# Optimization experiments

Measured on AMD Instinct MI355X. Metric: run time of the kernel, lower is better.

The kernel has to match this reference:

```python
import jax, jax.numpy as jnp
import numpy as np

B = 16          # number of trees (batch)
H = 256         # hidden_size == feature_size
S = 16          # Tree.num_sem
C = 5           # max_child_num (complete C-ary tree)
L = 6           # tree depth: leaves at level L, internal levels 0..L-1
N_LEAF = C**L                     # 15625
N_INT = (C**L - 1) // (C - 1)     # 3906 internal nodes, level-l offset = (C^l-1)/(C-1)


def setup_inputs() -> dict:
    key = jax.random.key(0)
    ks = jax.random.split(key, 20)
    rn = lambda k, shp, s=0.05: jax.random.normal(k, shp, dtype=jnp.float32) * s
    return {
        "leaf_box": jax.random.normal(ks[0], (B, N_LEAF, 4), dtype=jnp.float32),
        "leaf_sem": jax.random.uniform(ks[1], (B, N_LEAF, S), dtype=jnp.float32),
        "internal_box": jax.random.normal(ks[2], (B, N_INT, 4), dtype=jnp.float32),
        "node_type": jax.random.randint(ks[3], (B, N_INT), 0, 3, dtype=jnp.int32),
        "eps": jax.random.normal(ks[4], (B, H), dtype=jnp.float32),
        "W_box": rn(ks[5], (4, H)), "b_box": jnp.zeros((H,), jnp.float32),
        "W_sem": rn(ks[6], (S, H)), "b_sem": jnp.zeros((H,), jnp.float32),
        "W_node": rn(ks[7], (3, C * H, H)), "b_node": jnp.zeros((3, H), jnp.float32),
        "W1": rn(ks[8], (H, H)), "b1": jnp.zeros((H,), jnp.float32),
        "Wmu": rn(ks[9], (H, H)), "bmu": jnp.zeros((H,), jnp.float32),
        "Wvar": rn(ks[10], (H, H)), "bvar": jnp.zeros((H,), jnp.float32),
    }


def reference(leaf_box, leaf_sem, internal_box, node_type, eps,
              W_box, b_box, W_sem, b_sem, W_node, b_node,
              W1, b1, Wmu, bmu, Wvar, bvar):
    box_enc = lambda b: jax.nn.relu(b @ W_box + b_box)
    # LeafEncoder: relu-box-encoding + relu-sem-encoding
    feats = box_enc(leaf_box) + jax.nn.relu(leaf_sem @ W_sem + b_sem)  # [B, N_LEAF, H]
    # Bottom-up over internal levels (static loop over L=6 levels)
    for l in range(L - 1, -1, -1):
        n = C ** l
        off = (C ** l - 1) // (C - 1)
        child = feats.reshape(B, n, C * H)  # children flattened per parent (child_exists==1)
        # Apply all 3 branch encoders (vertical/horizontal/stack), select by node label
        y_all = jnp.einsum('bnk,tkh->bnth', child, W_node) + b_node          # [B,n,3,H]
        sel = jax.nn.one_hot(node_type[:, off:off + n], 3, dtype=child.dtype)  # [B,n,3]
        y = jnp.einsum('bnth,bnt->bnh', y_all, sel)
        feats = jax.nn.relu(y) + box_enc(internal_box[:, off:off + n])
    root = feats[:, 0]  # [B, H]
    # Sampler (variational, probabilistic)
    enc = jax.nn.relu(root @ W1 + b1)
    mu = enc @ Wmu + bmu
    logvar = enc @ Wvar + bvar
    std = jnp.exp(0.5 * logvar)
    kld = 1.0 + logvar - mu ** 2 - jnp.exp(logvar)
    return jnp.concatenate([eps * std + mu, kld], axis=1)  # [B, 2H]
```

## Files before the change

### kernel.cpp

```cpp
#include <hip/hip_runtime.h>


#define B_ 16
#define H_ 256
#define NLEAF 15625
#define NINT 3906
#define RND128(x) (((x) + 127) & ~127)
#define MEGA_NBLK 474

typedef __bf16 bf16_t;
typedef bf16_t bf16x8 __attribute__((ext_vector_type(8)));
typedef bf16_t bf16x4 __attribute__((ext_vector_type(4)));
typedef float f32x4 __attribute__((ext_vector_type(4)));

__device__ __forceinline__ void gl2lds16(const bf16_t* g, bf16_t* l) {
  __builtin_amdgcn_global_load_lds((const __attribute__((address_space(1))) void*)g,
                                   (__attribute__((address_space(3))) void*)l,
                                   16, 0, 0);
}

__global__ __launch_bounds__(256) void prep_kernel(const float* __restrict__ W_node,
                                                   bf16_t* __restrict__ Wt,
                                                   int* __restrict__ counters) {
  if (blockIdx.x == 0 && (threadIdx.x < 18 || (threadIdx.x >= 64 && threadIdx.x < 70)))
    counters[threadIdx.x] = 0;
  const int t = blockIdx.x / 80;
  const int kc = blockIdx.x % 80;
  const int h = threadIdx.x;
  const int half = h >> 7, r = h & 127;
  const int sw = (r >> 1) & 3;
  const float* srcp = W_node + (size_t)t * 1280 * 256 + h;
  bf16_t* base = Wt + ((size_t)(t * 2 + half) * 40) * 4096 + r * 32;
#pragma unroll
  for (int k0 = kc * 16; k0 < kc * 16 + 16; k0 += 8) {
    bf16x8 v;
#pragma unroll
    for (int j = 0; j < 8; ++j) v[j] = (bf16_t)srcp[(size_t)(k0 + j) * 256];
    const int ks = k0 >> 5;
    const int q = (k0 >> 3) & 3;
    *(bf16x8*)(base + (size_t)ks * 4096 + ((q ^ sw) << 3)) = v;
  }
}

__global__ __launch_bounds__(256) void bucket_kernel(const int* __restrict__ node_type,
                                                     int* __restrict__ counters,
                                                     int2* __restrict__ buckets) {
  __shared__ int lcnt[18];
  __shared__ int lbase[18];
  const int tid = threadIdx.x;
  if (tid < 18) lcnt[tid] = 0;
  __syncthreads();

  int idx = blockIdx.x * 256 + tid;
  bool active = idx < B_ * NINT;
  int t = 0, key = 0, mypos = 0;
  int2 e;
  int base = 0, nl_cap = 0;
  if (active) {
    int b = idx / NINT;
    int j = idx - b * NINT;
    int l, off;
    if (j >= 781)      { l = 5; off = 781; }
    else if (j >= 156) { l = 4; off = 156; }
    else if (j >= 31)  { l = 3; off = 31; }
    else if (j >= 6)   { l = 2; off = 6; }
    else if (j >= 1)   { l = 1; off = 1; }
    else               { l = 0; off = 0; }
    const int n_tab[6]    = {1, 5, 25, 125, 625, 3125};
    const int nn_tab[6]   = {5, 25, 125, 625, 3125, 15625};
    const int base_tab[6] = {0, 48, 288, 1488, 7488, 37488};
    int n_l = n_tab[l], nn = nn_tab[l];
    t = node_type[idx];
    int i = j - off;
    e.x = b * n_l + i;
    e.y = b * nn + 5 * i;
    base = base_tab[l];
    nl_cap = B_ * n_l;
    key = l * 3 + t;
    mypos = atomicAdd(&lcnt[key], 1);
  }
  __syncthreads();
  if (tid < 18) {
    int c = lcnt[tid];
    lbase[tid] = c ? atomicAdd(&counters[tid], c) : 0;
  }
  __syncthreads();
  if (active) {
    buckets[base + t * nl_cap + lbase[key] + mypos] = e;
  }
}

__global__ __launch_bounds__(256) void dest_kernel(const int2* __restrict__ buckets,
                                                   const int* __restrict__ counters,
                                                   int* __restrict__ wdest_all,
                                                   int* __restrict__ rsrc6) {
  int flat = blockIdx.x * 256 + threadIdx.x;
  if (flat >= 187488) return;
  int l, base, cap, coff;
  if (flat >= 37488)      { l = 5; base = 37488; cap = 50000; coff = 0; }
  else if (flat >= 7488)  { l = 4; base = 7488;  cap = 10000; coff = 12480; }
  else if (flat >= 1488)  { l = 3; base = 1488;  cap = 2000;  coff = 2480; }
  else if (flat >= 288)   { l = 2; base = 288;   cap = 400;   coff = 480; }
  else if (flat >= 48)    { l = 1; base = 48;    cap = 80;    coff = 80; }
  else                    { l = 0; base = 0;     cap = 16;    coff = 0; }
  int rel = flat - base;
  int t = (rel >= 2 * cap) ? 2 : (rel >= cap ? 1 : 0);
  int s = rel - t * cap;
  const int* c3 = counters + l * 3;
  if (s >= c3[t]) return;
  int pfxr = (t > 0 ? RND128(c3[0]) : 0) + (t > 1 ? RND128(c3[1]) : 0);
  int R = pfxr + s;
  int2 e = buckets[flat];
  if (l == 5) {
    int* rp = rsrc6 + 5 * R;
#pragma unroll
    for (int c = 0; c < 5; ++c) rp[c] = e.y + c;
  } else {
    int* wp = wdest_all + coff + 5 * e.x;
#pragma unroll
    for (int c = 0; c < 5; ++c) wp[c] = (R << 3) + c;
  }
}

__global__ __launch_bounds__(256) void leaf_kernel(
    const float* __restrict__ leaf_box, const float* __restrict__ leaf_sem,
    const float* __restrict__ W_box, const float* __restrict__ b_box,
    const float* __restrict__ W_sem, const float* __restrict__ b_sem,
    const int* __restrict__ rsrc, bf16_t* __restrict__ g5) {
  const int lane = threadIdx.x & 63;
  const int wave = threadIdx.x >> 6;
  const int q = lane >> 4;
  const int c = lane & 15;
  const int hh = wave & 1;
  const int gw = wave >> 1;

  bf16x8 wsem[8], wbox[8];
#pragma unroll
  for (int T = 0; T < 8; ++T) {
    const int hb = (hh * 8 + T) * 16 + c;
    bf16x8 a;
#pragma unroll
    for (int j = 0; j < 8; ++j) a[j] = (bf16_t)0.f;
    if (q < 2) {
#pragma unroll
      for (int j = 0; j < 8; ++j) a[j] = (bf16_t)W_sem[(q * 8 + j) * H_ + hb];
    } else if (q == 2) {
      a[0] = (bf16_t)b_sem[hb];
    }
    wsem[T] = a;
    bf16x8 b;
#pragma unroll
    for (int j = 0; j < 8; ++j) b[j] = (bf16_t)0.f;
    if (q == 0) {
#pragma unroll
      for (int j = 0; j < 4; ++j) b[j] = (bf16_t)W_box[j * H_ + hb];
      b[4] = (bf16_t)b_box[hb];
    }
    wbox[T] = b;
  }

  const int NG2 = 15705;
  const int gstride = gridDim.x * 2;
  for (int g = blockIdx.x * 2 + gw; g < NG2; g += gstride) {
    const int ci = g * 16 + c;
    int row = rsrc[ci];
    row = ((unsigned)row < (unsigned)(B_ * NLEAF)) ? row : 0;
    const int R = ci / 5;
    const int c5 = ci - R * 5;
    bf16x8 xs, xb;
#pragma unroll
    for (int j = 0; j < 8; ++j) { xs[j] = (bf16_t)0.f; xb[j] = (bf16_t)0.f; }
    if (q < 2) {
      const float4* sp = (const float4*)(leaf_sem + (size_t)row * 16 + q * 8);
      float4 s0 = sp[0], s1 = sp[1];
      xs[0] = (bf16_t)s0.x; xs[1] = (bf16_t)s0.y; xs[2] = (bf16_t)s0.z; xs[3] = (bf16_t)s0.w;
      xs[4] = (bf16_t)s1.x; xs[5] = (bf16_t)s1.y; xs[6] = (bf16_t)s1.z; xs[7] = (bf16_t)s1.w;
    } else if (q == 2) {
      xs[0] = (bf16_t)1.0f;
    }
    if (q == 0) {
      float4 bx = *(const float4*)(leaf_box + (size_t)row * 4);
      xb[0] = (bf16_t)bx.x; xb[1] = (bf16_t)bx.y; xb[2] = (bf16_t)bx.z; xb[3] = (bf16_t)bx.w;
      xb[4] = (bf16_t)1.0f;
    }
    const int rr = R & 127;
    const int sw = (rr >> 1) & 3;
    bf16_t* obase = g5 + (size_t)(R >> 7) * 163840 + rr * 32;
#pragma unroll
    for (int T = 0; T < 8; ++T) {
      f32x4 z = {0.f, 0.f, 0.f, 0.f};
      f32x4 as = __builtin_amdgcn_mfma_f32_16x16x32_bf16(wsem[T], xs, z, 0, 0, 0);
      f32x4 ab = __builtin_amdgcn_mfma_f32_16x16x32_bf16(wbox[T], xb, z, 0, 0, 0);
      bf16x4 o;
#pragma unroll
      for (int r = 0; r < 4; ++r)
        o[r] = (bf16_t)(fmaxf(as[r], 0.f) + fmaxf(ab[r], 0.f));
      const int ks = c5 * 8 + hh * 4 + (T >> 1);
      const int pc = (((T & 1) << 1) | (q >> 1)) ^ sw;
      *(bf16x4*)(obase + (size_t)ks * 4096 + (pc << 3) + ((q & 1) << 2)) = o;
    }
  }
}

__device__ __forceinline__ void level_phase(
    int x, const bf16_t* __restrict__ src, bf16_t* __restrict__ dst,
    const int2* __restrict__ bucket, const int* __restrict__ counters,
    const bf16_t* __restrict__ Wt, const float* __restrict__ b_node,
    const float* __restrict__ ibox, const float* __restrict__ W_box,
    const float* __restrict__ b_box, const int* __restrict__ wdest,
    int n_l, int off_l, int cap, int P,
    bf16_t Asm[3][128][32], bf16_t Bsm[3][128][32]) {
  if (x >= 6 * P) return;
  const int t = x / (2 * P);
  const int r2 = x - t * 2 * P;
  const int nblk = r2 / P;
  const int p = r2 - nblk * P;
  const int cnt = counters[t];
  const int tile0 = p * 128;
  if (tile0 >= cnt) return;
  const int pfxr = (t > 0 ? RND128(counters[0]) : 0) + (t > 1 ? RND128(counters[1]) : 0);
  const int2* rd = bucket + (size_t)t * cap;

  const int tid = threadIdx.x;
  const int lane = tid & 63;
  const int wave = tid >> 6;
  const int wm = wave & 1, wn = wave >> 1;
  const int quad = lane >> 4;
  const int l15 = lane & 15;

  const bf16_t* ga0 = src + (size_t)(pfxr + tile0) * 1280 + wave * 1024 + (lane << 3);
  const bf16_t* gb0 = Wt + ((size_t)(t * 2 + nblk) * 40) * 4096 + wave * 1024 + (lane << 3);

  f32x4 acc[4][4];
#pragma unroll
  for (int i = 0; i < 4; ++i)
#pragma unroll
    for (int j = 0; j < 4; ++j) acc[i][j] = (f32x4){0.f, 0.f, 0.f, 0.f};

  const int pcs = (quad ^ ((l15 >> 1) & 3)) * 8;

#define STG2(buf, ks)                                   \
  {                                                     \
    const bf16_t* ga = ga0 + (ks) * 4096;               \
    const bf16_t* gb = gb0 + (ks) * 4096;               \
    bf16_t* la = &Asm[buf][0][0] + wave * 1024;         \
    bf16_t* lb = &Bsm[buf][0][0] + wave * 1024;         \
    gl2lds16(ga, la);                                   \
    gl2lds16(ga + 512, la + 512);                       \
    gl2lds16(gb, lb);                                   \
    gl2lds16(gb + 512, lb + 512);                       \
  }
#define FRG2(bufv)                                                            \
  {                                                                           \
    bf16x8 af[4], bfr[4];                                                     \
    _Pragma("unroll") for (int am = 0; am < 4; ++am)                          \
        af[am] = *(const bf16x8*)(&Asm[bufv][wm * 64 + am * 16 + l15][pcs]);  \
    _Pragma("unroll") for (int bn = 0; bn < 4; ++bn)                          \
        bfr[bn] = *(const bf16x8*)(&Bsm[bufv][wn * 64 + bn * 16 + l15][pcs]); \
    __builtin_amdgcn_s_setprio(1);                                            \
    _Pragma("unroll") for (int am = 0; am < 4; ++am)                          \
        _Pragma("unroll") for (int bn = 0; bn < 4; ++bn)                      \
            acc[am][bn] = __builtin_amdgcn_mfma_f32_16x16x32_bf16(            \
                af[am], bfr[bn], acc[am][bn], 0, 0, 0);                       \
    __builtin_amdgcn_s_setprio(0);                                            \
  }

  STG2(0, 0)
  STG2(1, 1)
  int rbuf = 0, wbuf = 2;
  for (int ks = 0; ks < 38; ++ks) {
    asm volatile("s_waitcnt vmcnt(4)" ::: "memory");
    __builtin_amdgcn_s_barrier();
    {
      bf16x8 af[4], bfr[4];
#pragma unroll
      for (int am = 0; am < 4; ++am)
        af[am] = *(const bf16x8*)(&Asm[rbuf][wm * 64 + am * 16 + l15][pcs]);
#pragma unroll
      for (int bn = 0; bn < 4; ++bn)
        bfr[bn] = *(const bf16x8*)(&Bsm[rbuf][wn * 64 + bn * 16 + l15][pcs]);
      STG2(wbuf, ks + 2)
      __builtin_amdgcn_s_setprio(1);
#pragma unroll
      for (int am = 0; am < 4; ++am)
#pragma unroll
        for (int bn = 0; bn < 4; ++bn)
          acc[am][bn] = __builtin_amdgcn_mfma_f32_16x16x32_bf16(af[am], bfr[bn], acc[am][bn], 0, 0, 0);
      __builtin_amdgcn_s_setprio(0);
    }
    rbuf = (rbuf + 1 == 3) ? 0 : rbuf + 1;
    wbuf = (wbuf + 1 == 3) ? 0 : wbuf + 1;
  }
  asm volatile("s_waitcnt vmcnt(4)" ::: "memory");
  __builtin_amdgcn_s_barrier();
  FRG2(rbuf)
  rbuf = (rbuf + 1 == 3) ? 0 : rbuf + 1;
  asm volatile("s_waitcnt vmcnt(0)" ::: "memory");
  __builtin_amdgcn_s_barrier();
  FRG2(rbuf)
#undef FRG2
#undef STG2

  float wbv[4][6];
#pragma unroll
  for (int bn = 0; bn < 4; ++bn) {
    int col = nblk * 128 + wn * 64 + bn * 16 + l15;
    wbv[bn][0] = W_box[col];
    wbv[bn][1] = W_box[H_ + col];
    wbv[bn][2] = W_box[2 * H_ + col];
    wbv[bn][3] = W_box[3 * H_ + col];
    wbv[bn][4] = b_box[col];
    wbv[bn][5] = b_node[t * H_ + col];
  }
#pragma unroll
  for (int am = 0; am < 4; ++am) {
    int orw_[4]; float4 bxv[4]; bool valid[4];
#pragma unroll
    for (int r = 0; r < 4; ++r) {
      int gidx = tile0 + wm * 64 + am * 16 + quad * 4 + r;
      valid[r] = (gidx < cnt);
      int ic = valid[r] ? gidx : (cnt - 1);
      int orw = rd[ic].x;
      orw_[r] = orw;
      int b = orw / n_l;
      int i = orw - b * n_l;
      bxv[r] = *(const float4*)(ibox + ((size_t)b * NINT + off_l + i) * 4);
    }
    if (wdest) {
      size_t ob[4]; int sw_[4];
#pragma unroll
      for (int r = 0; r < 4; ++r) {
        int wd = wdest[orw_[r]];
        int R = wd >> 3, cc = wd & 7;
        int rr = R & 127;
        ob[r] = (size_t)(R >> 7) * 163840 + (size_t)cc * 32768 + (size_t)rr * 32;
        sw_[r] = (rr >> 1) & 3;
      }
#pragma unroll
      for (int bn = 0; bn < 4; ++bn) {
        int col = nblk * 128 + wn * 64 + bn * 16 + l15;
        int kc2 = col >> 5, qq = (col >> 3) & 3, ww = col & 7;
#pragma unroll
        for (int r = 0; r < 4; ++r) {
          if (!valid[r]) continue;
          float y = fmaxf(acc[am][bn][r] + wbv[bn][5], 0.f);
          float be = fmaf(wbv[bn][0], bxv[r].x,
                     fmaf(wbv[bn][1], bxv[r].y,
                     fmaf(wbv[bn][2], bxv[r].z,
                     fmaf(wbv[bn][3], bxv[r].w, wbv[bn][4]))));
          be = fmaxf(be, 0.f);
          dst[ob[r] + (size_t)kc2 * 4096 + ((qq ^ sw_[r]) << 3) + ww] = (bf16_t)(y + be);
        }
      }
    } else {
#pragma unroll
      for (int bn = 0; bn < 4; ++bn) {
        int col = nblk * 128 + wn * 64 + bn * 16 + l15;
#pragma unroll
        for (int r = 0; r < 4; ++r) {
          if (!valid[r]) continue;
          float y = fmaxf(acc[am][bn][r] + wbv[bn][5], 0.f);
          float be = fmaf(wbv[bn][0], bxv[r].x,
                     fmaf(wbv[bn][1], bxv[r].y,
                     fmaf(wbv[bn][2], bxv[r].z,
                     fmaf(wbv[bn][3], bxv[r].w, wbv[bn][4]))));
          be = fmaxf(be, 0.f);
          dst[(size_t)orw_[r] * H_ + col] = (bf16_t)(y + be);
        }
      }
    }
  }
}

__global__ __launch_bounds__(256) void level5_kernel(
    const bf16_t* __restrict__ src, bf16_t* __restrict__ dst,
    const int2* __restrict__ bucket, const int* __restrict__ counters,
    const bf16_t* __restrict__ Wt, const float* __restrict__ b_node,
    const float* __restrict__ ibox, const float* __restrict__ W_box,
    const float* __restrict__ b_box, const int* __restrict__ wdest,
    int n_l, int off_l, int cap) {
  __shared__ __align__(16) bf16_t Asm[3][128][32];
  __shared__ __align__(16) bf16_t Bsm[3][128][32];
  const int x = blockIdx.x;
  const int p = ((x >> 4) << 3) + (x & 7);
  const int nblk = (x >> 3) & 1;
  const int t = blockIdx.y;
  const int P = gridDim.x / 2;
  const int xx = t * 2 * P + nblk * P + p;
  level_phase(xx, src, dst, bucket, counters, Wt, b_node, ibox, W_box, b_box,
              wdest, n_l, off_l, cap, P, Asm, Bsm);
}

__device__ __forceinline__ void grid_barrier(int* bar, int ph, int expect) {
  __syncthreads();
  if (threadIdx.x == 0) {
    __threadfence();
    __hip_atomic_fetch_add(&bar[ph], 1, __ATOMIC_RELAXED, __HIP_MEMORY_SCOPE_AGENT);
    while (__hip_atomic_load(&bar[ph], __ATOMIC_RELAXED, __HIP_MEMORY_SCOPE_AGENT) < expect)
      __builtin_amdgcn_s_sleep(8);
    __threadfence();
  }
  __syncthreads();
}

struct MegaArgs {
  const bf16_t* src[5];
  bf16_t* dst[5];
  const int2* buckets;
  const int* counters;
  int* bar;
  const int* wdest_all;
  const bf16_t* Wt;
  const float* b_node;
  const float* ibox;
  const float* W_box;
  const float* b_box;
  const bf16_t* f0;
  const float* eps;
  const float* W1;
  const float* b1;
  const float* Wmu;
  const float* bmu;
  const float* Wvar;
  const float* bvar;
  float* out;
};

__global__ __launch_bounds__(256, 2) void mega_kernel(MegaArgs a) {
  __shared__ __align__(16) bf16_t Asm[3][128][32];
  __shared__ __align__(16) bf16_t Bsm[3][128][32];
  __shared__ float hroot[256];
  __shared__ float henc[256];
  constexpr int BKT_OFF[5] = {7488, 1488, 288, 48, 0};
  constexpr int CNT_OFF[5] = {12, 9, 6, 3, 0};
  constexpr int WOFF[5]    = {2480, 480, 80, 0, -1};
  constexpr int NL[5]      = {625, 125, 25, 5, 1};
  constexpr int OFFL[5]    = {156, 31, 6, 1, 0};
  constexpr int CAP[5]     = {10000, 2000, 400, 80, 16};
  constexpr int PAIRS[5]   = {79, 16, 4, 1, 1};
  constexpr int EXPECT[5]     = {474, 96, 24, 16, 16};
  constexpr int NEED_AFTER[5] = {96, 24, 16, 16, 16};
  const int x = blockIdx.x;
#pragma unroll
  for (int li = 0; li < 5; ++li) {
    const int* wd = (li == 4) ? nullptr : (a.wdest_all + WOFF[li]);
    level_phase(x, a.src[li], a.dst[li], a.buckets + BKT_OFF[li],
                a.counters + CNT_OFF[li], a.Wt, a.b_node, a.ibox, a.W_box,
                a.b_box, wd, NL[li], OFFL[li], CAP[li], PAIRS[li], Asm, Bsm);
    grid_barrier(a.bar, li, EXPECT[li]);
    if (x >= NEED_AFTER[li]) return;
  }
  if (x < 16) {
    const int b = x, h = threadIdx.x;
    hroot[h] = (float)a.f0[b * H_ + h];
    __syncthreads();
    float v = a.b1[h];
    for (int k = 0; k < 256; ++k) v = fmaf(hroot[k], a.W1[k * H_ + h], v);
    henc[h] = fmaxf(v, 0.f);
    __syncthreads();
    float m = a.bmu[h], lv = a.bvar[h];
    for (int k = 0; k < 256; ++k) {
      float e = henc[k];
      m = fmaf(e, a.Wmu[k * H_ + h], m);
      lv = fmaf(e, a.Wvar[k * H_ + h], lv);
    }
    float stdv = expf(0.5f * lv);
    float kld = 1.f + lv - m * m - expf(lv);
    a.out[b * 512 + h] = a.eps[b * H_ + h] * stdv + m;
    a.out[b * 512 + 256 + h] = kld;
  }
}

extern "C" void kernel_launch(void* const* d_in, const int* in_sizes, int n_in,
                              void* d_out, int out_size, void* d_ws, size_t ws_size,
                              hipStream_t stream) {
  const float* leaf_box     = (const float*)d_in[0];
  const float* leaf_sem     = (const float*)d_in[1];
  const float* internal_box = (const float*)d_in[2];
  const int*   node_type    = (const int*)d_in[3];
  const float* eps          = (const float*)d_in[4];
  const float* W_box        = (const float*)d_in[5];
  const float* b_box        = (const float*)d_in[6];
  const float* W_sem        = (const float*)d_in[7];
  const float* b_sem        = (const float*)d_in[8];
  const float* W_node       = (const float*)d_in[9];
  const float* b_node       = (const float*)d_in[10];
  const float* W1           = (const float*)d_in[11];
  const float* b1           = (const float*)d_in[12];
  const float* Wmu          = (const float*)d_in[13];
  const float* bmu          = (const float*)d_in[14];
  const float* Wvar         = (const float*)d_in[15];
  const float* bvar         = (const float*)d_in[16];
  float* out = (float*)d_out;

  char* p = (char*)d_ws;
  auto alloc = [&](size_t bytes) {
    char* r = p;
    p += (bytes + 255) & ~(size_t)255;
    return r;
  };
  const int n_tab[6] = {1, 5, 25, 125, 625, 3125};
  bf16_t* Wt = (bf16_t*)alloc((size_t)3 * 2 * 40 * 4096 * 2);
  bf16_t* f0 = (bf16_t*)alloc((size_t)B_ * H_ * 2);
  bf16_t* G[6];
  for (int l = 0; l <= 5; ++l)
    G[l] = (bf16_t*)alloc(((size_t)B_ * n_tab[l] + 384) * 1280 * 2);
  int* counters  = (int*)alloc(128 * 4);
  int2* buckets  = (int2*)alloc((size_t)187488 * 8);
  int* wdest_all = (int*)alloc((size_t)62480 * 4);
  int* rsrc6     = (int*)alloc((size_t)251280 * 4);

  hipLaunchKernelGGL(prep_kernel, dim3(240), dim3(256), 0, stream, W_node, Wt, counters);
  hipLaunchKernelGGL(bucket_kernel, dim3((B_ * NINT + 255) / 256), dim3(256), 0, stream,
                     node_type, counters, buckets);
  hipLaunchKernelGGL(dest_kernel, dim3((187488 + 255) / 256), dim3(256), 0, stream,
                     buckets, counters, wdest_all, rsrc6);
  hipLaunchKernelGGL(leaf_kernel, dim3(1024), dim3(256), 0, stream,
                     leaf_box, leaf_sem, W_box, b_box, W_sem, b_sem, rsrc6, G[5]);

  {
    int cap = B_ * n_tab[5];
    int tiles = (cap + 127) / 128;
    int tiles8 = (tiles + 7) & ~7;
    hipLaunchKernelGGL(level5_kernel, dim3(2 * tiles8, 3), dim3(256), 0, stream,
                       G[5], G[4], buckets + 37488, counters + 15,
                       Wt, b_node, internal_box, W_box, b_box,
                       wdest_all + 12480, 3125, 781, cap);
  }

  {
    MegaArgs ma;
    ma.src[0] = G[4]; ma.dst[0] = G[3];
    ma.src[1] = G[3]; ma.dst[1] = G[2];
    ma.src[2] = G[2]; ma.dst[2] = G[1];
    ma.src[3] = G[1]; ma.dst[3] = G[0];
    ma.src[4] = G[0]; ma.dst[4] = f0;
    ma.buckets = buckets; ma.counters = counters; ma.bar = counters + 64;
    ma.wdest_all = wdest_all;
    ma.Wt = Wt; ma.b_node = b_node; ma.ibox = internal_box;
    ma.W_box = W_box; ma.b_box = b_box;
    ma.f0 = f0; ma.eps = eps; ma.W1 = W1; ma.b1 = b1;
    ma.Wmu = Wmu; ma.bmu = bmu; ma.Wvar = Wvar; ma.bvar = bvar; ma.out = out;
    hipLaunchKernelGGL(mega_kernel, dim3(MEGA_NBLK), dim3(256), 0, stream, ma);
  }
}
```

Before: 413.7 us.

## Replace LDS-tiled level GEMM in persistent kernel with 16-row direct-load MFMA slices

Result: slower. 505.9 us (+22.3%).

```diff
diff --git a/kernel.cpp b/kernel.cpp
--- a/kernel.cpp
+++ b/kernel.cpp
@@ -396,7 +396,9 @@
   if (threadIdx.x == 0) {
     __threadfence();
     __hip_atomic_fetch_add(&bar[ph], 1, __ATOMIC_RELAXED, __HIP_MEMORY_SCOPE_AGENT);
-    while (__hip_atomic_load(&bar[ph], __ATOMIC_RELAXED, __HIP_MEMORY_SCOPE_AGENT) < expect)
+    int guard = 0;
+    while (__hip_atomic_load(&bar[ph], __ATOMIC_RELAXED, __HIP_MEMORY_SCOPE_AGENT) < expect &&
+           ++guard < (1 << 24))
       __builtin_amdgcn_s_sleep(8);
     __threadfence();
   }
@@ -427,8 +429,6 @@
 };
 
 __global__ __launch_bounds__(256, 2) void mega_kernel(MegaArgs a) {
-  __shared__ __align__(16) bf16_t Asm[3][128][32];
-  __shared__ __align__(16) bf16_t Bsm[3][128][32];
   __shared__ float hroot[256];
   __shared__ float henc[256];
   constexpr int BKT_OFF[5] = {7488, 1488, 288, 48, 0};
@@ -437,18 +437,121 @@
   constexpr int NL[5]      = {625, 125, 25, 5, 1};
   constexpr int OFFL[5]    = {156, 31, 6, 1, 0};
   constexpr int CAP[5]     = {10000, 2000, 400, 80, 16};
-  constexpr int PAIRS[5]   = {79, 16, 4, 1, 1};
-  constexpr int EXPECT[5]     = {474, 96, 24, 16, 16};
-  constexpr int NEED_AFTER[5] = {96, 24, 16, 16, 16};
+  constexpr int TP[5]      = {625, 125, 25, 5, 1};
+  constexpr int ALIVE[5]   = {474, 375, 75, 16, 16};
+  constexpr int NEED[5]    = {375, 75, 16, 16, 16};
+
   const int x = blockIdx.x;
+  const int tid = threadIdx.x;
+  const int lane = tid & 63;
+  const int wave = tid >> 6;
+  const int quad = lane >> 4;
+  const int l15 = lane & 15;
+  const int pcs = (quad ^ ((l15 >> 1) & 3)) * 8;
+
+  int cols[4];
+  float wb0[4], wb1[4], wb2[4], wb3[4], wb4[4];
+  const bf16_t* bp0[4];
+#pragma unroll
+  for (int bn = 0; bn < 4; ++bn) {
+    int col = wave * 64 + bn * 16 + l15;
+    cols[bn] = col;
+    wb0[bn] = a.W_box[col];
+    wb1[bn] = a.W_box[H_ + col];
+    wb2[bn] = a.W_box[2 * H_ + col];
+    wb3[bn] = a.W_box[3 * H_ + col];
+    wb4[bn] = a.b_box[col];
+    bp0[bn] = a.Wt + (size_t)(col >> 7) * 163840 + (col & 127) * 32 + pcs;
+  }
+
 #pragma unroll
   for (int li = 0; li < 5; ++li) {
-    const int* wd = (li == 4) ? nullptr : (a.wdest_all + WOFF[li]);
-    level_phase(x, a.src[li], a.dst[li], a.buckets + BKT_OFF[li],
-                a.counters + CNT_OFF[li], a.Wt, a.b_node, a.ibox, a.W_box,
-                a.b_box, wd, NL[li], OFFL[li], CAP[li], PAIRS[li], Asm, Bsm);
-    grid_barrier(a.bar, li, EXPECT[li]);
-    if (x >= NEED_AFTER[li]) return;
+    const int* cnts = a.counters + CNT_OFF[li];
+    const int c0 = cnts[0], c1 = cnts[1], c2v = cnts[2];
+    for (int sl = x; sl < 3 * TP[li]; sl += ALIVE[li]) {
+      const int t = sl / TP[li];
+      const int s = sl - t * TP[li];
+      const int cnt = (t == 0) ? c0 : (t == 1 ? c1 : c2v);
+      const int tile0 = s * 16;
+      if (tile0 >= cnt) continue;
+      const int pfxr = (t > 0 ? RND128(c0) : 0) + (t > 1 ? RND128(c1) : 0);
+      const int2* rd = a.buckets + BKT_OFF[li] + (size_t)t * CAP[li];
+      const int Rbase = pfxr + tile0;
+      const bf16_t* aptr = a.src[li] + (size_t)(Rbase >> 7) * 163840 +
+                           ((Rbase & 127) + l15) * 32 + pcs;
+      const size_t toff = (size_t)t * 327680;
+      f32x4 acc[4];
+#pragma unroll
+      for (int bn = 0; bn < 4; ++bn) acc[bn] = (f32x4){0.f, 0.f, 0.f, 0.f};
+#pragma unroll 4
+      for (int ks = 0; ks < 40; ++ks) {
+        bf16x8 af = *(const bf16x8*)(aptr + (size_t)ks * 4096);
+#pragma unroll
+        for (int bn = 0; bn < 4; ++bn) {
+          bf16x8 bfr = *(const bf16x8*)(bp0[bn] + toff + (size_t)ks * 4096);
+          acc[bn] = __builtin_amdgcn_mfma_f32_16x16x32_bf16(af, bfr, acc[bn], 0, 0, 0);
+        }
+      }
+      int orw_[4]; float4 bxv[4]; bool valid[4];
+#pragma unroll
+      for (int r = 0; r < 4; ++r) {
+        int gidx = tile0 + quad * 4 + r;
+        valid[r] = (gidx < cnt);
+        int ic = valid[r] ? gidx : (cnt - 1);
+        int orw = rd[ic].x;
+        orw_[r] = orw;
+        int b = orw / NL[li];
+        int i = orw - b * NL[li];
+        bxv[r] = *(const float4*)(a.ibox + ((size_t)b * NINT + OFFL[li] + i) * 4);
+      }
+      if (li < 4) {
+        const int* wdest = a.wdest_all + WOFF[li];
+        size_t ob[4]; int swz[4];
+#pragma unroll
+        for (int r = 0; r < 4; ++r) {
+          int wd = wdest[orw_[r]];
+          int R = wd >> 3, cc = wd & 7;
+          int rr = R & 127;
+          ob[r] = (size_t)(R >> 7) * 163840 + (size_t)cc * 32768 + (size_t)rr * 32;
+          swz[r] = (rr >> 1) & 3;
+        }
+        bf16_t* dst = a.dst[li];
+#pragma unroll
+        for (int bn = 0; bn < 4; ++bn) {
+          int col = cols[bn];
+          float bn5 = a.b_node[t * H_ + col];
+          int kc2 = col >> 5, qq = (col >> 3) & 3, ww = col & 7;
+#pragma unroll
+          for (int r = 0; r < 4; ++r) {
+            if (!valid[r]) continue;
+            float y = fmaxf(acc[bn][r] + bn5, 0.f);
+            float be = fmaf(wb0[bn], bxv[r].x, fmaf(wb1[bn], bxv[r].y,
+                       fmaf(wb2[bn], bxv[r].z, fmaf(wb3[bn], bxv[r].w, wb4[bn]))));
+            be = fmaxf(be, 0.f);
+            dst[ob[r] + (size_t)kc2 * 4096 + ((size_t)(qq ^ swz[r]) << 3) + ww] =
+                (bf16_t)(y + be);
+          }
+        }
+      } else {
+        bf16_t* dst = a.dst[li];
+#pragma unroll
+        for (int bn = 0; bn < 4; ++bn) {
+          int col = cols[bn];
+          float bn5 = a.b_node[t * H_ + col];
+#pragma unroll
+          for (int r = 0; r < 4; ++r) {
+            if (!valid[r]) continue;
+            float y = fmaxf(acc[bn][r] + bn5, 0.f);
+            float be = fmaf(wb0[bn], bxv[r].x, fmaf(wb1[bn], bxv[r].y,
+                       fmaf(wb2[bn], bxv[r].z, fmaf(wb3[bn], bxv[r].w, wb4[bn]))));
+            be = fmaxf(be, 0.f);
+            dst[(size_t)orw_[r] * H_ + col] = (bf16_t)(y + be);
+          }
+        }
+      }
+    }
+    grid_barrier(a.bar, li, ALIVE[li]);
+    if (li < 4 && x >= NEED[li]) return;
   }
   if (x < 16) {
     const int b = x, h = threadIdx.x;
```
